# Kernel optimization log

Hardware: AMD Instinct MI355X
Metric: run time of the kernel (lower is better)

## Reference

```python
import jax, jax.numpy as jnp
import numpy as np

N_BINS = 18
EPS = 1e-9


def setup_inputs() -> dict:
    key = jax.random.key(0)
    k1, k2 = jax.random.split(key)
    # pha: phase values in [-pi, pi], shape (B, C, Fp, S, T)
    pha = jax.random.uniform(k1, (4, 16, 10, 4, 2048), dtype=jnp.float32,
                             minval=-np.pi, maxval=np.pi)
    # amp: non-negative amplitude envelope, shape (B, C, Fa, S, T)
    amp = jax.random.uniform(k2, (4, 16, 30, 4, 2048), dtype=jnp.float32)
    return {"pha": pha, "amp": amp}


def reference(pha, amp):
    # Bin cutoffs: linspace(-pi, pi, n_bins+1), matching the torch buffer.
    cutoffs = jnp.linspace(-np.pi, np.pi, N_BINS + 1, dtype=jnp.float32)
    # torch.bucketize(right=False) == searchsorted side='left'; then -1, clamp.
    bins = jnp.clip(jnp.searchsorted(cutoffs, pha, side='left') - 1, 0, N_BINS - 1)
    # One-hot mask over phase bins: (B, C, Fp, S, T, K)
    onehot = jax.nn.one_hot(bins, N_BINS, dtype=amp.dtype)
    # Per-bin amplitude sums, contracting over time t (avoids the torch 7D tensor):
    # amp_sums[b,c,p,a,s,k] = sum_t onehot[b,c,p,s,t,k] * amp[b,c,a,s,t]
    amp_sums = jnp.einsum('bcpstk,bcast->bcpask', onehot, amp)  # (B,C,Fp,Fa,S,K)
    counts = onehot.sum(axis=4)  # (B, C, Fp, S, K)
    amp_means = amp_sums / (counts[:, :, :, None] + EPS)  # broadcast over Fa
    amp_probs = amp_means / (amp_means.sum(axis=-1, keepdims=True) + EPS)
    # Negative entropy term over bins: (B, C, Fp, Fa, S)
    ent = (amp_probs * jnp.log(amp_probs + EPS)).sum(axis=-1)
    MI = (jnp.log(N_BINS + EPS) + ent) / jnp.log(jnp.float32(N_BINS))
    # Mean over segments -> (B, C, Fp, Fa)
    return MI.mean(axis=-1)
```

## Files before the change

### kernel.cpp

```cpp
#include <hip/hip_runtime.h>
#include <math.h>


#define FP_ 10
#define FA_ 30
#define K_  18
#define T_  2048
#define TC_ 512
#define NTILE 4
#define RS_ 260
#define NT_ 512

typedef _Float16 half8 __attribute__((ext_vector_type(8)));
typedef float    f32x4 __attribute__((ext_vector_type(4)));

#define LDS_BYTES (128 + 20480 + 33280 + 33280 + 50688)

__global__ __launch_bounds__(NT_, 2)
void mi_main(const float* __restrict__ pha, const float* __restrict__ amp,
             float* __restrict__ ws) {
  extern __shared__ unsigned char smem[];
  float*    c_lds = (float*)smem;
  unsigned* binsw = (unsigned*)(smem + 128);
  unsigned* amp_h = (unsigned*)(smem + 128 + 20480);
  unsigned* amp_l = (unsigned*)(smem + 128 + 20480 + 33280);
  float*    red   = (float*)(smem + 128 + 20480 + 66560);

  const int tid  = threadIdx.x;
  const int lane = tid & 63;
  const int wv   = tid >> 6;
  const int quad = lane >> 4;
  const int lc   = lane & 15;
  const int q    = wv >> 1;
  const int gh   = wv & 1;

  const int g  = blockIdx.x;
  const int s  = g & 3;
  const int bc = g >> 2;
  const long pha_base = (long)bc * (FP_ * 4L * T_) + (long)s * T_;
  const long amp_base = (long)bc * (FA_ * 4L * T_) + (long)s * T_;

  if (tid < 19) {
    const double PI_D = 3.14159265358979323846264338327950288;
    const double step = (2.0 * PI_D) / 18.0;
    c_lds[tid] = (tid == 18) ? (float)PI_D : (float)(-PI_D + (double)tid * step);
  }
  for (int i = tid; i < RS_; i += NT_) {
    amp_h[30 * RS_ + i] = 0x3C003C00u;
    amp_h[31 * RS_ + i] = 0u;
    amp_l[30 * RS_ + i] = 0u;
    amp_l[31 * RS_ + i] = 0u;
  }
  __syncthreads();

  const float PI_F    = 3.14159274101257324f;
  const float INVSTEP = 2.8647890f;
  #pragma unroll
  for (int p = 0; p < FP_; ++p) {
    const float4 v = *(const float4*)(pha + pha_base + (long)p * (4L * T_) + tid * 4);
    float xs[4] = {v.x, v.y, v.z, v.w};
    unsigned pk = 0;
    #pragma unroll
    for (int j = 0; j < 4; ++j) {
      const float x = xs[j];
      int gi = (int)((x + PI_F) * INVSTEP);
      gi = min(17, max(0, gi));
      if (x <= c_lds[gi]) gi -= 1;
      else if (x > c_lds[gi + 1]) gi += 1;
      gi = min(17, max(0, gi));
      pk |= ((unsigned)gi) << (8 * j);
    }
    binsw[p * 512 + tid] = pk;
  }

  const bool stager = tid < 480;
  const int a_row = tid >> 4;
  const int seg   = tid & 15;
  const float* gsrc = amp + amp_base + (long)a_row * (4L * T_) + seg * 32;
  float4 vreg[8];
  if (stager) {
    #pragma unroll
    for (int j = 0; j < 8; ++j) vreg[j] = *(const float4*)(gsrc + j * 4);
  }

  f32x4 acch[6][2], accl[6][2];
  #pragma unroll
  for (int mt = 0; mt < 6; ++mt) {
    acch[mt][0] = (f32x4){0.f,0.f,0.f,0.f}; acch[mt][1] = (f32x4){0.f,0.f,0.f,0.f};
    accl[mt][0] = (f32x4){0.f,0.f,0.f,0.f}; accl[mt][1] = (f32x4){0.f,0.f,0.f,0.f};
  }

  for (int tile = 0; tile < NTILE; ++tile) {
    if (stager) {
      unsigned hw[16], lw[16];
      #pragma unroll
      for (int j = 0; j < 8; ++j) {
        const float xv[4] = {vreg[j].x, vreg[j].y, vreg[j].z, vreg[j].w};
        #pragma unroll
        for (int e = 0; e < 4; e += 2) {
          _Float16 h0 = (_Float16)xv[e];
          _Float16 h1 = (_Float16)xv[e + 1];
          _Float16 l0 = (_Float16)((xv[e]     - (float)h0) * 4096.0f);
          _Float16 l1 = (_Float16)((xv[e + 1] - (float)h1) * 4096.0f);
          const unsigned uh0 = (unsigned)__builtin_bit_cast(unsigned short, h0);
          const unsigned uh1 = (unsigned)__builtin_bit_cast(unsigned short, h1);
          const unsigned ul0 = (unsigned)__builtin_bit_cast(unsigned short, l0);
          const unsigned ul1 = (unsigned)__builtin_bit_cast(unsigned short, l1);
          hw[j * 2 + e / 2] = uh0 | (uh1 << 16);
          lw[j * 2 + e / 2] = ul0 | (ul1 << 16);
        }
      }
      unsigned* dh = &amp_h[a_row * RS_ + seg * 16];
      unsigned* dl = &amp_l[a_row * RS_ + seg * 16];
      #pragma unroll
      for (int k4 = 0; k4 < 4; ++k4) {
        ((uint4*)dh)[k4] = make_uint4(hw[4*k4], hw[4*k4+1], hw[4*k4+2], hw[4*k4+3]);
        ((uint4*)dl)[k4] = make_uint4(lw[4*k4], lw[4*k4+1], lw[4*k4+2], lw[4*k4+3]);
      }
    }
    __syncthreads();
    if (stager && tile < NTILE - 1) {
      #pragma unroll
      for (int j = 0; j < 8; ++j)
        vreg[j] = *(const float4*)(gsrc + (tile + 1) * TC_ + j * 4);
    }

    #pragma unroll
    for (int ci = 0; ci < 4; ++ci) {
      const int cl   = q * 4 + ci;
      const int boff = cl * 16 + quad * 4;
      const half8 bh0 = __builtin_bit_cast(half8, *(const uint4*)&amp_h[lc * RS_ + boff]);
      const half8 bh1 = __builtin_bit_cast(half8, *(const uint4*)&amp_h[(16 + lc) * RS_ + boff]);
      const half8 bl0 = __builtin_bit_cast(half8, *(const uint4*)&amp_l[lc * RS_ + boff]);
      const half8 bl1 = __builtin_bit_cast(half8, *(const uint4*)&amp_l[(16 + lc) * RS_ + boff]);
      const int wbase = tile * 128 + cl * 8 + quad * 2;
      #pragma unroll
      for (int mt = 0; mt < 6; ++mt) {
        const int row = gh * 96 + mt * 16 + lc;
        int p = row / 18;  p = min(p, 9);
        const unsigned kb = (unsigned)(row - p * 18);
        const uint2 w01 = *(const uint2*)&binsw[p * 512 + wbase];
        unsigned aw[4];
        #pragma unroll
        for (int j2 = 0; j2 < 4; ++j2) {
          const unsigned w  = (j2 < 2) ? w01.x : w01.y;
          const unsigned sh = (unsigned)(j2 & 1) * 16u;
          const unsigned b0 = (w >> sh) & 0xFFu;
          const unsigned b1 = (w >> (sh + 8u)) & 0xFFu;
          aw[j2] = (b0 == kb ? 0x3C00u : 0u) | (b1 == kb ? 0x3C000000u : 0u);
        }
        const half8 af = __builtin_bit_cast(half8, make_uint4(aw[0], aw[1], aw[2], aw[3]));
        acch[mt][0] = __builtin_amdgcn_mfma_f32_16x16x32_f16(af, bh0, acch[mt][0], 0, 0, 0);
        accl[mt][0] = __builtin_amdgcn_mfma_f32_16x16x32_f16(af, bl0, accl[mt][0], 0, 0, 0);
        acch[mt][1] = __builtin_amdgcn_mfma_f32_16x16x32_f16(af, bh1, acch[mt][1], 0, 0, 0);
        accl[mt][1] = __builtin_amdgcn_mfma_f32_16x16x32_f16(af, bl1, accl[mt][1], 0, 0, 0);
      }
    }
    __syncthreads();
  }

  f32x4 acc[6][2];
  #pragma unroll
  for (int mt = 0; mt < 6; ++mt) {
    acc[mt][0] = acch[mt][0] + accl[mt][0] * 2.44140625e-4f;
    acc[mt][1] = acch[mt][1] + accl[mt][1] * 2.44140625e-4f;
  }

  float* slotA = &red[(gh * 2 + (q & 1)) * 96 * 33];
  (void)slotA;
  {
    #define STORE48(S) do { \
      _Pragma("unroll") for (int mt = 0; mt < 6; ++mt) \
      _Pragma("unroll") for (int n = 0; n < 2; ++n) \
      _Pragma("unroll") for (int r = 0; r < 4; ++r) \
        (S)[(mt * 16 + quad * 4 + r) * 33 + n * 16 + lc] = acc[mt][n][r]; } while (0)
    #define ADD48(S) do { \
      _Pragma("unroll") for (int mt = 0; mt < 6; ++mt) \
      _Pragma("unroll") for (int n = 0; n < 2; ++n) \
      _Pragma("unroll") for (int r = 0; r < 4; ++r) \
        acc[mt][n][r] += (S)[(mt * 16 + quad * 4 + r) * 33 + n * 16 + lc]; } while (0)

    if (q >= 2) { float* S = &red[(gh * 2 + (q - 2)) * 96 * 33]; STORE48(S); }
    __syncthreads();
    if (q < 2)  { float* S = &red[(gh * 2 + q) * 96 * 33];       ADD48(S); }
    __syncthreads();
    if (q == 1) { float* S = &red[(gh * 2) * 96 * 33];           STORE48(S); }
    __syncthreads();
    if (q == 0) { float* S = &red[(gh * 2) * 96 * 33];           ADD48(S); }
    __syncthreads();
    if (q == 0) {
      #pragma unroll
      for (int mt = 0; mt < 6; ++mt)
        #pragma unroll
        for (int n = 0; n < 2; ++n)
          #pragma unroll
          for (int r = 0; r < 4; ++r)
            red[(gh * 96 + mt * 16 + quad * 4 + r) * 33 + n * 16 + lc] = acc[mt][n][r];
    }
    __syncthreads();
  }

  if (tid < FP_ * FA_) {
    const int p = tid / FA_;
    const int a = tid - p * FA_;
    float m[K_];
    float tot = 0.0f;
    #pragma unroll
    for (int k = 0; k < K_; ++k) {
      const float cnt = red[(p * K_ + k) * 33 + 30];
      const float sv  = red[(p * K_ + k) * 33 + a];
      const float mk  = sv / (cnt + 1e-9f);
      m[k] = mk;
      tot += mk;
    }
    const float denom = tot + 1e-9f;
    float ent = 0.0f;
    #pragma unroll
    for (int k = 0; k < K_; ++k) {
      const float pr = m[k] / denom;
      ent += pr * logf(pr + 1e-9f);
    }
    const float L  = logf(18.0f);
    const float mi = (L + ent) / L;
    ws[(((long)bc * FP_ + p) * FA_ + a) * 4 + s] = mi;
  }
}

__global__ __launch_bounds__(256)
void mi_reduce(const float* __restrict__ ws, float* __restrict__ out) {
  const int i = blockIdx.x * 256 + threadIdx.x;
  if (i < 4 * 16 * FP_ * FA_) {
    const float* w = ws + (long)i * 4;
    out[i] = (((w[0] + w[1]) + w[2]) + w[3]) * 0.25f;
  }
}

extern "C" void kernel_launch(void* const* d_in, const int* in_sizes, int n_in,
                              void* d_out, int out_size, void* d_ws, size_t ws_size,
                              hipStream_t stream) {
  const float* pha = (const float*)d_in[0];
  const float* amp = (const float*)d_in[1];
  float* out = (float*)d_out;
  float* ws  = (float*)d_ws;

  static bool attr_set = false;
  if (!attr_set) {
    hipFuncSetAttribute((const void*)mi_main,
                        hipFuncAttributeMaxDynamicSharedMemorySize, LDS_BYTES);
    attr_set = true;
  }
  hipLaunchKernelGGL(mi_main, dim3(256), dim3(NT_), LDS_BYTES, stream, pha, amp, ws);
  hipLaunchKernelGGL(mi_reduce, dim3((19200 + 255) / 256), dim3(256), 0, stream, ws, out);
}
```

Before: 124.0 us.

## Split time axis across two blocks per segment and move entropy to second kernel

Each (b,c,s) group is now handled by two blocks, each covering half the time axis, so the grid doubles to 512 blocks. The per-block LDS footprint shrinks (reduction buffer overlays the bins buffer), allowing launch bounds of 4 blocks per CU for higher occupancy. Warps are reassigned so each covers 48 rows with fewer accumulators and a single-stage cross-warp reduction, and bins are packed as 16-bit values so the one-hot fragments come from packed 16-bit compares. Partial bin sums go to workspace, and a new second kernel combines the halves, computes the entropy and averages over segments, which adds workspace traffic.

```diff
diff --git a/kernel.cpp b/kernel.cpp
--- a/kernel.cpp
+++ b/kernel.cpp
@@ -6,39 +6,52 @@
 #define FA_ 30
 #define K_  18
 #define T_  2048
-#define TC_ 512
+#define TH_ 1024
+#define TC_ 256
 #define NTILE 4
-#define RS_ 260
+#define RS_ 132
+#define BS_ 516
 #define NT_ 512
 
 typedef _Float16 half8 __attribute__((ext_vector_type(8)));
 typedef float    f32x4 __attribute__((ext_vector_type(4)));
-
-#define LDS_BYTES (128 + 20480 + 33280 + 33280 + 50688)
-
-__global__ __launch_bounds__(NT_, 2)
+typedef unsigned short u16x2 __attribute__((ext_vector_type(2)));
+typedef short          s16x2 __attribute__((ext_vector_type(2)));
+
+#define LDS_BYTES 54560
+
+static __device__ __forceinline__ unsigned onehot2(unsigned w, unsigned kk) {
+  const u16x2 x  = __builtin_bit_cast(u16x2, w ^ kk);
+  const s16x2 eq = (s16x2)(x == (u16x2)(unsigned short)0);
+  const u16x2 m  = __builtin_bit_cast(u16x2, eq) & (u16x2)(unsigned short)0x3C00;
+  return __builtin_bit_cast(unsigned, m);
+}
+
+__global__ __launch_bounds__(NT_, 4)
 void mi_main(const float* __restrict__ pha, const float* __restrict__ amp,
              float* __restrict__ ws) {
   extern __shared__ unsigned char smem[];
   float*    c_lds = (float*)smem;
   unsigned* binsw = (unsigned*)(smem + 128);
-  unsigned* amp_h = (unsigned*)(smem + 128 + 20480);
-  unsigned* amp_l = (unsigned*)(smem + 128 + 20480 + 33280);
-  float*    red   = (float*)(smem + 128 + 20480 + 66560);
+  unsigned* amp_h = (unsigned*)(smem + 20768);
+  unsigned* amp_l = (unsigned*)(smem + 37664);
+  float*    red   = (float*)(smem + 128);
 
   const int tid  = threadIdx.x;
   const int lane = tid & 63;
   const int wv   = tid >> 6;
   const int quad = lane >> 4;
   const int lc   = lane & 15;
-  const int q    = wv >> 1;
-  const int gh   = wv & 1;
-
-  const int g  = blockIdx.x;
-  const int s  = g & 3;
-  const int bc = g >> 2;
-  const long pha_base = (long)bc * (FP_ * 4L * T_) + (long)s * T_;
-  const long amp_base = (long)bc * (FA_ * 4L * T_) + (long)s * T_;
+  const int mq   = wv & 3;
+  const int q2   = wv >> 2;
+
+  const int bid  = blockIdx.x;
+  const int g    = bid >> 1;
+  const int half = bid & 1;
+  const int s    = g & 3;
+  const int bc   = g >> 2;
+  const long pha_base = (long)bc * (FP_ * 4L * T_) + (long)s * T_ + half * TH_;
+  const long amp_base = (long)bc * (FA_ * 4L * T_) + (long)s * T_ + half * TH_;
 
   if (tid < 19) {
     const double PI_D = 3.14159265358979323846264338327950288;
@@ -53,48 +66,59 @@
   }
   __syncthreads();
 
+  int p_mt[3]; unsigned kk_mt[3];
+  #pragma unroll
+  for (int mt = 0; mt < 3; ++mt) {
+    const int row = mq * 48 + mt * 16 + lc;
+    int p = row / 18; p = min(p, 9);
+    const unsigned kb = (unsigned)(row - p * 18);
+    p_mt[mt] = p;
+    kk_mt[mt] = kb | (kb << 16);
+  }
+
   const float PI_F    = 3.14159274101257324f;
   const float INVSTEP = 2.8647890f;
   #pragma unroll
   for (int p = 0; p < FP_; ++p) {
-    const float4 v = *(const float4*)(pha + pha_base + (long)p * (4L * T_) + tid * 4);
-    float xs[4] = {v.x, v.y, v.z, v.w};
+    const float2 v = *(const float2*)(pha + pha_base + (long)p * (4L * T_) + tid * 2);
+    float xs[2] = {v.x, v.y};
     unsigned pk = 0;
     #pragma unroll
-    for (int j = 0; j < 4; ++j) {
+    for (int j = 0; j < 2; ++j) {
       const float x = xs[j];
       int gi = (int)((x + PI_F) * INVSTEP);
       gi = min(17, max(0, gi));
       if (x <= c_lds[gi]) gi -= 1;
       else if (x > c_lds[gi + 1]) gi += 1;
       gi = min(17, max(0, gi));
-      pk |= ((unsigned)gi) << (8 * j);
-    }
-    binsw[p * 512 + tid] = pk;
+      pk |= ((unsigned)gi) << (16 * j);
+    }
+    binsw[p * BS_ + tid] = pk;
   }
 
   const bool stager = tid < 480;
   const int a_row = tid >> 4;
   const int seg   = tid & 15;
-  const float* gsrc = amp + amp_base + (long)a_row * (4L * T_) + seg * 32;
-  float4 vreg[8];
+  const float* gsrc = amp + amp_base + (long)a_row * (4L * T_) + seg * 16;
+  float4 vreg[4];
   if (stager) {
     #pragma unroll
-    for (int j = 0; j < 8; ++j) vreg[j] = *(const float4*)(gsrc + j * 4);
-  }
-
-  f32x4 acch[6][2], accl[6][2];
-  #pragma unroll
-  for (int mt = 0; mt < 6; ++mt) {
+    for (int j = 0; j < 4; ++j) vreg[j] = *(const float4*)(gsrc + j * 4);
+  }
+
+  f32x4 acch[3][2], accl[3][2];
+  #pragma unroll
+  for (int mt = 0; mt < 3; ++mt) {
     acch[mt][0] = (f32x4){0.f,0.f,0.f,0.f}; acch[mt][1] = (f32x4){0.f,0.f,0.f,0.f};
     accl[mt][0] = (f32x4){0.f,0.f,0.f,0.f}; accl[mt][1] = (f32x4){0.f,0.f,0.f,0.f};
   }
+  __syncthreads();
 
   for (int tile = 0; tile < NTILE; ++tile) {
     if (stager) {
-      unsigned hw[16], lw[16];
-      #pragma unroll
-      for (int j = 0; j < 8; ++j) {
+      unsigned hw[8], lw[8];
+      #pragma unroll
+      for (int j = 0; j < 4; ++j) {
         const float xv[4] = {vreg[j].x, vreg[j].y, vreg[j].z, vreg[j].w};
         #pragma unroll
         for (int e = 0; e < 4; e += 2) {
@@ -102,54 +126,42 @@
           _Float16 h1 = (_Float16)xv[e + 1];
           _Float16 l0 = (_Float16)((xv[e]     - (float)h0) * 4096.0f);
           _Float16 l1 = (_Float16)((xv[e + 1] - (float)h1) * 4096.0f);
-          const unsigned uh0 = (unsigned)__builtin_bit_cast(unsigned short, h0);
-          const unsigned uh1 = (unsigned)__builtin_bit_cast(unsigned short, h1);
-          const unsigned ul0 = (unsigned)__builtin_bit_cast(unsigned short, l0);
-          const unsigned ul1 = (unsigned)__builtin_bit_cast(unsigned short, l1);
-          hw[j * 2 + e / 2] = uh0 | (uh1 << 16);
-          lw[j * 2 + e / 2] = ul0 | (ul1 << 16);
+          hw[j*2 + e/2] = (unsigned)__builtin_bit_cast(unsigned short, h0)
+                        | ((unsigned)__builtin_bit_cast(unsigned short, h1) << 16);
+          lw[j*2 + e/2] = (unsigned)__builtin_bit_cast(unsigned short, l0)
+                        | ((unsigned)__builtin_bit_cast(unsigned short, l1) << 16);
         }
       }
-      unsigned* dh = &amp_h[a_row * RS_ + seg * 16];
-      unsigned* dl = &amp_l[a_row * RS_ + seg * 16];
-      #pragma unroll
-      for (int k4 = 0; k4 < 4; ++k4) {
-        ((uint4*)dh)[k4] = make_uint4(hw[4*k4], hw[4*k4+1], hw[4*k4+2], hw[4*k4+3]);
-        ((uint4*)dl)[k4] = make_uint4(lw[4*k4], lw[4*k4+1], lw[4*k4+2], lw[4*k4+3]);
-      }
+      unsigned* dh = &amp_h[a_row * RS_ + seg * 8];
+      unsigned* dl = &amp_l[a_row * RS_ + seg * 8];
+      ((uint4*)dh)[0] = make_uint4(hw[0], hw[1], hw[2], hw[3]);
+      ((uint4*)dh)[1] = make_uint4(hw[4], hw[5], hw[6], hw[7]);
+      ((uint4*)dl)[0] = make_uint4(lw[0], lw[1], lw[2], lw[3]);
+      ((uint4*)dl)[1] = make_uint4(lw[4], lw[5], lw[6], lw[7]);
     }
     __syncthreads();
     if (stager && tile < NTILE - 1) {
       #pragma unroll
-      for (int j = 0; j < 8; ++j)
+      for (int j = 0; j < 4; ++j)
         vreg[j] = *(const float4*)(gsrc + (tile + 1) * TC_ + j * 4);
     }
 
     #pragma unroll
     for (int ci = 0; ci < 4; ++ci) {
-      const int cl   = q * 4 + ci;
+      const int cl   = q2 * 4 + ci;
       const int boff = cl * 16 + quad * 4;
       const half8 bh0 = __builtin_bit_cast(half8, *(const uint4*)&amp_h[lc * RS_ + boff]);
       const half8 bh1 = __builtin_bit_cast(half8, *(const uint4*)&amp_h[(16 + lc) * RS_ + boff]);
       const half8 bl0 = __builtin_bit_cast(half8, *(const uint4*)&amp_l[lc * RS_ + boff]);
       const half8 bl1 = __builtin_bit_cast(half8, *(const uint4*)&amp_l[(16 + lc) * RS_ + boff]);
-      const int wbase = tile * 128 + cl * 8 + quad * 2;
-      #pragma unroll
-      for (int mt = 0; mt < 6; ++mt) {
-        const int row = gh * 96 + mt * 16 + lc;
-        int p = row / 18;  p = min(p, 9);
-        const unsigned kb = (unsigned)(row - p * 18);
-        const uint2 w01 = *(const uint2*)&binsw[p * 512 + wbase];
-        unsigned aw[4];
-        #pragma unroll
-        for (int j2 = 0; j2 < 4; ++j2) {
-          const unsigned w  = (j2 < 2) ? w01.x : w01.y;
-          const unsigned sh = (unsigned)(j2 & 1) * 16u;
-          const unsigned b0 = (w >> sh) & 0xFFu;
-          const unsigned b1 = (w >> (sh + 8u)) & 0xFFu;
-          aw[j2] = (b0 == kb ? 0x3C00u : 0u) | (b1 == kb ? 0x3C000000u : 0u);
-        }
-        const half8 af = __builtin_bit_cast(half8, make_uint4(aw[0], aw[1], aw[2], aw[3]));
+      const int widx = tile * 128 + cl * 16 + quad * 4;
+      #pragma unroll
+      for (int mt = 0; mt < 3; ++mt) {
+        const uint4 wb = *(const uint4*)&binsw[p_mt[mt] * BS_ + widx];
+        const unsigned kk = kk_mt[mt];
+        const half8 af = __builtin_bit_cast(half8,
+            make_uint4(onehot2(wb.x, kk), onehot2(wb.y, kk),
+                       onehot2(wb.z, kk), onehot2(wb.w, kk)));
         acch[mt][0] = __builtin_amdgcn_mfma_f32_16x16x32_f16(af, bh0, acch[mt][0], 0, 0, 0);
         accl[mt][0] = __builtin_amdgcn_mfma_f32_16x16x32_f16(af, bl0, accl[mt][0], 0, 0, 0);
         acch[mt][1] = __builtin_amdgcn_mfma_f32_16x16x32_f16(af, bh1, acch[mt][1], 0, 0, 0);
@@ -159,56 +171,58 @@
     __syncthreads();
   }
 
-  f32x4 acc[6][2];
-  #pragma unroll
-  for (int mt = 0; mt < 6; ++mt) {
+  f32x4 acc[3][2];
+  #pragma unroll
+  for (int mt = 0; mt < 3; ++mt) {
     acc[mt][0] = acch[mt][0] + accl[mt][0] * 2.44140625e-4f;
     acc[mt][1] = acch[mt][1] + accl[mt][1] * 2.44140625e-4f;
   }
 
-  float* slotA = &red[(gh * 2 + (q & 1)) * 96 * 33];
-  (void)slotA;
-  {
-    #define STORE48(S) do { \
-      _Pragma("unroll") for (int mt = 0; mt < 6; ++mt) \
-      _Pragma("unroll") for (int n = 0; n < 2; ++n) \
-      _Pragma("unroll") for (int r = 0; r < 4; ++r) \
-        (S)[(mt * 16 + quad * 4 + r) * 33 + n * 16 + lc] = acc[mt][n][r]; } while (0)
-    #define ADD48(S) do { \
-      _Pragma("unroll") for (int mt = 0; mt < 6; ++mt) \
-      _Pragma("unroll") for (int n = 0; n < 2; ++n) \
-      _Pragma("unroll") for (int r = 0; r < 4; ++r) \
-        acc[mt][n][r] += (S)[(mt * 16 + quad * 4 + r) * 33 + n * 16 + lc]; } while (0)
-
-    if (q >= 2) { float* S = &red[(gh * 2 + (q - 2)) * 96 * 33]; STORE48(S); }
-    __syncthreads();
-    if (q < 2)  { float* S = &red[(gh * 2 + q) * 96 * 33];       ADD48(S); }
-    __syncthreads();
-    if (q == 1) { float* S = &red[(gh * 2) * 96 * 33];           STORE48(S); }
-    __syncthreads();
-    if (q == 0) { float* S = &red[(gh * 2) * 96 * 33];           ADD48(S); }
-    __syncthreads();
-    if (q == 0) {
-      #pragma unroll
-      for (int mt = 0; mt < 6; ++mt)
+  if (q2 == 1) {
+    float* S = &red[mq * 48 * 33];
+    #pragma unroll
+    for (int mt = 0; mt < 3; ++mt)
+      #pragma unroll
+      for (int n = 0; n < 2; ++n)
         #pragma unroll
-        for (int n = 0; n < 2; ++n)
-          #pragma unroll
-          for (int r = 0; r < 4; ++r)
-            red[(gh * 96 + mt * 16 + quad * 4 + r) * 33 + n * 16 + lc] = acc[mt][n][r];
-    }
-    __syncthreads();
-  }
-
-  if (tid < FP_ * FA_) {
-    const int p = tid / FA_;
-    const int a = tid - p * FA_;
+        for (int r = 0; r < 4; ++r)
+          S[(mt * 16 + quad * 4 + r) * 33 + n * 16 + lc] = acc[mt][n][r];
+  }
+  __syncthreads();
+  if (q2 == 0) {
+    float* S = &red[mq * 48 * 33];
+    float* W = ws + (long)bid * 6144;
+    #pragma unroll
+    for (int mt = 0; mt < 3; ++mt)
+      #pragma unroll
+      for (int n = 0; n < 2; ++n)
+        #pragma unroll
+        for (int r = 0; r < 4; ++r) {
+          const float v = acc[mt][n][r] + S[(mt * 16 + quad * 4 + r) * 33 + n * 16 + lc];
+          W[(mq * 48 + mt * 16 + quad * 4 + r) * 32 + n * 16 + lc] = v;
+        }
+  }
+}
+
+__global__ __launch_bounds__(320)
+void mi_ent(const float* __restrict__ ws, float* __restrict__ out) {
+  const int bc = blockIdx.x;
+  const int t  = threadIdx.x;
+  if (t >= FP_ * FA_) return;
+  const int p = t / FA_;
+  const int a = t - p * FA_;
+  const float L = logf(18.0f);
+  float mi_sum = 0.0f;
+  for (int s = 0; s < 4; ++s) {
+    const float* w0 = ws + ((long)(bc * 4 + s) * 2) * 6144;
+    const float* w1 = w0 + 6144;
     float m[K_];
     float tot = 0.0f;
     #pragma unroll
     for (int k = 0; k < K_; ++k) {
-      const float cnt = red[(p * K_ + k) * 33 + 30];
-      const float sv  = red[(p * K_ + k) * 33 + a];
+      const int r = (p * K_ + k) * 32;
+      const float cnt = w0[r + 30] + w1[r + 30];
+      const float sv  = w0[r + a]  + w1[r + a];
       const float mk  = sv / (cnt + 1e-9f);
       m[k] = mk;
       tot += mk;
@@ -220,19 +234,9 @@
       const float pr = m[k] / denom;
       ent += pr * logf(pr + 1e-9f);
     }
-    const float L  = logf(18.0f);
-    const float mi = (L + ent) / L;
-    ws[(((long)bc * FP_ + p) * FA_ + a) * 4 + s] = mi;
-  }
-}
-
-__global__ __launch_bounds__(256)
-void mi_reduce(const float* __restrict__ ws, float* __restrict__ out) {
-  const int i = blockIdx.x * 256 + threadIdx.x;
-  if (i < 4 * 16 * FP_ * FA_) {
-    const float* w = ws + (long)i * 4;
-    out[i] = (((w[0] + w[1]) + w[2]) + w[3]) * 0.25f;
-  }
+    mi_sum += (L + ent) / L;
+  }
+  out[bc * (FP_ * FA_) + t] = mi_sum * 0.25f;
 }
 
 extern "C" void kernel_launch(void* const* d_in, const int* in_sizes, int n_in,
@@ -249,6 +253,6 @@
                         hipFuncAttributeMaxDynamicSharedMemorySize, LDS_BYTES);
     attr_set = true;
   }
-  hipLaunchKernelGGL(mi_main, dim3(256), dim3(NT_), LDS_BYTES, stream, pha, amp, ws);
-  hipLaunchKernelGGL(mi_reduce, dim3((19200 + 255) / 256), dim3(256), 0, stream, ws, out);
-}
+  hipLaunchKernelGGL(mi_main, dim3(512), dim3(NT_), LDS_BYTES, stream, pha, amp, ws);
+  hipLaunchKernelGGL(mi_ent, dim3(64), dim3(320), 0, stream, ws, out);
+}
```

After: 143.3 us. 15.5% more time.
